# Kernel optimization log

Hardware: AMD Instinct MI355X
Metric: run time of the kernel (lower is better)

The kernel has to match this reference:

```python
import jax, jax.numpy as jnp
import numpy as np

NUM_ITER = 3
HEADS = 8
EPS = 1e-8

def _ln(x, g, b, eps=1e-5):
    mu = x.mean(-1, keepdims=True)
    var = ((x - mu) ** 2).mean(-1, keepdims=True)
    return (x - mu) * jax.lax.rsqrt(var + eps) * g + b

def setup_inputs() -> dict:
    key = jax.random.key(0)
    ks = jax.random.split(key, 10)
    B, Nkv, Din = 32, 4096, 256
    Nq, S, Hm = 16, 256, 512
    def xav(k, shape):
        lim = (6.0 / (shape[0] + shape[1])) ** 0.5
        return jax.random.uniform(k, shape, minval=-lim, maxval=lim, dtype=jnp.float32)
    return {
        "slots": jax.random.normal(ks[0], (Nq, S), dtype=jnp.float32),
        "inputs": jax.random.normal(ks[1], (B, Nkv, Din), dtype=jnp.float32),
        "norm_in_g": jnp.ones((Din,), jnp.float32), "norm_in_b": jnp.zeros((Din,), jnp.float32),
        "norm_slots_g": jnp.ones((S,), jnp.float32), "norm_slots_b": jnp.zeros((S,), jnp.float32),
        "norm_mlp_g": jnp.ones((S,), jnp.float32), "norm_mlp_b": jnp.zeros((S,), jnp.float32),
        "Wq": xav(ks[2], (S, S)), "Wk": xav(ks[3], (S, Din)), "Wv": xav(ks[4], (S, Din)),
        "gru_wih": xav(ks[5], (3 * S, S)),
        "gru_whh": jax.random.normal(ks[6], (3 * S, S), dtype=jnp.float32) * (1.0 / S ** 0.5),
        "gru_bih": jnp.zeros((3 * S,), jnp.float32), "gru_bhh": jnp.zeros((3 * S,), jnp.float32),
        "mlp_w1": xav(ks[7], (Hm, S)), "mlp_b1": jnp.zeros((Hm,), jnp.float32),
        "mlp_w2": xav(ks[8], (S, Hm)), "mlp_b2": jnp.zeros((S,), jnp.float32),
    }

def reference(slots, inputs, norm_in_g, norm_in_b, norm_slots_g, norm_slots_b,
              norm_mlp_g, norm_mlp_b, Wq, Wk, Wv, gru_wih, gru_whh, gru_bih, gru_bhh,
              mlp_w1, mlp_b1, mlp_w2, mlp_b2):
    B, Nkv, Din = inputs.shape
    Nq, S = slots.shape
    H = HEADS
    hd = S // H
    slots = jnp.broadcast_to(slots, (B, Nq, S))
    x = _ln(inputs, norm_in_g, norm_in_b)
    k = (x @ Wk.T).reshape(B, Nkv, H, hd).transpose(0, 2, 1, 3) * (hd ** -0.5)  # [B,H,Nkv,hd]
    v = (x @ Wv.T).reshape(B, Nkv, H, hd).transpose(0, 2, 1, 3)
    attn_vis = None
    for _ in range(NUM_ITER):
        slots_prev = slots
        s = _ln(slots, norm_slots_g, norm_slots_b)
        q = (s @ Wq.T).reshape(B, Nq, H, hd).transpose(0, 2, 1, 3)  # [B,H,Nq,hd]
        # logits [B,Nkv,H*Nq]; softmax jointly over heads and slots per key (slot-axis softmax)
        logits = jnp.einsum('bhkd,bhqd->bkhq', k, q).reshape(B, Nkv, H * Nq)
        attn = jax.nn.softmax(logits, axis=-1).reshape(B, Nkv, H, Nq).transpose(0, 2, 1, 3)  # [B,H,Nkv,Nq]
        attn_vis = attn.sum(1)  # [B,Nkv,Nq]
        attn_n = attn / (attn.sum(axis=2, keepdims=True) + EPS)  # normalize over keys
        updates = jnp.einsum('bhkq,bhkd->bqhd', attn_n, v).reshape(B, Nq, S)
        # GRUCell: gates order r,z,n
        xg = updates.reshape(-1, S)
        h = slots_prev.reshape(-1, S)
        gi = xg @ gru_wih.T + gru_bih
        gh = h @ gru_whh.T + gru_bhh
        ir, iz, inn = jnp.split(gi, 3, axis=-1)
        hr, hz, hn = jnp.split(gh, 3, axis=-1)
        r = jax.nn.sigmoid(ir + hr)
        z = jax.nn.sigmoid(iz + hz)
        n = jnp.tanh(inn + r * hn)
        slots = ((1.0 - z) * n + z * h).reshape(B, Nq, S)
        m = _ln(slots, norm_mlp_g, norm_mlp_b)
        slots = slots + (jax.nn.relu(m @ mlp_w1.T + mlp_b1) @ mlp_w2.T + mlp_b2)
    return (slots, attn_vis)
```

## Files before the change

### kernel.cpp

```cpp
#include <hip/hip_runtime.h>
#include <stdint.h>

typedef unsigned short u16;
typedef __attribute__((ext_vector_type(8))) _Float16 half8;
typedef __attribute__((ext_vector_type(4))) _Float16 half4;
typedef __attribute__((ext_vector_type(4))) float floatx4;

__device__ inline float bflo(unsigned u){ return __uint_as_float(u << 16); }
__device__ inline float bfhi(unsigned u){ return __uint_as_float(u & 0xffff0000u); }
__device__ inline float bf1(u16 v){ return __uint_as_float(((unsigned)v) << 16); }
__device__ inline u16 f2bf(float f){
  unsigned u = __float_as_uint(f);
  u += 0x7fffu + ((u >> 16) & 1u);
  return (u16)(u >> 16);
}
__device__ inline float dot8(uint4 w, float4 a, float4 b, float acc){
  acc = fmaf(bflo(w.x), a.x, acc); acc = fmaf(bfhi(w.x), a.y, acc);
  acc = fmaf(bflo(w.y), a.z, acc); acc = fmaf(bfhi(w.y), a.w, acc);
  acc = fmaf(bflo(w.z), b.x, acc); acc = fmaf(bfhi(w.z), b.y, acc);
  acc = fmaf(bflo(w.w), b.z, acc); acc = fmaf(bfhi(w.w), b.w, acc);
  return acc;
}

#define CW_SLOTS 0
#define CW_GIN   4096
#define CW_BIN   4352
#define CW_GS    4608
#define CW_BS    4864
#define CW_GM    5120
#define CW_BM    5376
#define CW_WQ    5632
#define CW_WK    71168
#define CW_WV    136704
#define CW_WIH   202240
#define CW_WHH   398848
#define CW_BIH   595456
#define CW_BHH   596224
#define CW_W1    596992
#define CW_B1    728064
#define CW_W2    728576
#define CW_B2    859648
#define CW_TOTAL 859904

__global__ void k_flag(const u16* __restrict__ probe, int* __restrict__ flag){
  int t = threadIdx.x;
  int bad = 0;
  #pragma unroll
  for (int i = 0; i < 4; i++){
    float x = bf1(probe[t + i * 256]);
    if (!(fabsf(x) < 1e6f)) bad = 1;
  }
  __shared__ int s;
  if (t == 0) s = 0;
  __syncthreads();
  if (bad) atomicOr(&s, 1);
  __syncthreads();
  if (t == 0) *flag = s;
}

struct CanonArgs { const void* p[18]; };

__global__ void k_canon(CanonArgs a, const int* __restrict__ flag, u16* __restrict__ cw){
  const int off[19] = {CW_SLOTS, CW_GIN, CW_BIN, CW_GS, CW_BS, CW_GM, CW_BM, CW_WQ,
                       CW_WK, CW_WV, CW_WIH, CW_WHH, CW_BIH, CW_BHH, CW_W1, CW_B1,
                       CW_W2, CW_B2, CW_TOTAL};
  int i = blockIdx.x * 256 + threadIdx.x;
  if (i >= CW_TOTAL) return;
  int f32m = *flag;
  int j = 0;
  while (i >= off[j + 1]) j++;
  int local = i - off[j];
  float v = f32m ? ((const float*)a.p[j])[local] : bf1(((const u16*)a.p[j])[local]);
  cw[i] = f2bf(v);
}

__global__ void k_init(const u16* __restrict__ cw, float* __restrict__ slots,
                       _Float16* __restrict__ wkvh)
{
  int idx = blockIdx.x * 256 + threadIdx.x;
  if (idx < 131072){
    float g = bf1(cw[CW_GIN + (idx & 255)]);
    wkvh[idx] = (_Float16)(bf1(cw[CW_WK + idx]) * g);
  } else {
    int i = idx - 131072;
    int d = i & 255;
    int q = (i >> 8) & 15;
    slots[i] = bf1(cw[CW_SLOTS + q * 256 + d]);
  }
}

__global__ void k_beta(const u16* __restrict__ cw, float* __restrict__ beta,
                       float* __restrict__ colsum){
  int c = blockIdx.x * 256 + threadIdx.x;
  if (c >= 512) return;
  float a = 0.f, s = 0.f;
  for (int d = 0; d < 256; d++){
    float w = bf1(cw[CW_WK + c * 256 + d]);
    a = fmaf(bf1(cw[CW_BIN + d]), w, a);
    s = fmaf(bf1(cw[CW_GIN + d]), w, s);
  }
  beta[c] = a;
  colsum[c] = s;
}

__global__ void k_zero(float* __restrict__ p, int n){
  int i = blockIdx.x * 256 + threadIdx.x;
  if (i < n) p[i] = 0.f;
}

__global__ __launch_bounds__(256) void k1_gemm(
    const void* __restrict__ inp, const int* __restrict__ flag,
    const float* __restrict__ beta, const float* __restrict__ colsum,
    const _Float16* __restrict__ wkvh, _Float16* __restrict__ kh, _Float16* __restrict__ vT)
{
  int f32m = *flag;
  int tid = threadIdx.x;
  int wv = tid >> 6, lane = tid & 63;
  int m16 = lane & 15, q4 = lane >> 4;
  int nb = blockIdx.y;
  long rowb0 = (long)blockIdx.x * 128;
  int colW = nb * 256 + wv * 64;

  __shared__ _Float16 vtile[256][72];

  half8 bfr[4][8];
  #pragma unroll
  for (int nt = 0; nt < 4; nt++)
    #pragma unroll
    for (int s = 0; s < 8; s++)
      bfr[nt][s] = *(const half8*)(wkvh + (colW + nt * 16 + m16) * 256 + s * 32 + q4 * 8);

  float bet[4], cs[4];
  #pragma unroll
  for (int nt = 0; nt < 4; nt++){
    bet[nt] = beta[colW + nt * 16 + m16];
    cs[nt]  = colsum[colW + nt * 16 + m16];
  }

  for (int rt = 0; rt < 8; rt++){
    long rowb = rowb0 + rt * 16;
    long myRow = rowb + m16;

    float sum = 0.f, sq = 0.f;
    half8 af[8];
    if (f32m){
      const float* rp = (const float*)inp + myRow * 256 + q4 * 8;
      #pragma unroll
      for (int s = 0; s < 8; s++){
        float4 x0 = *(const float4*)(rp + s * 32);
        float4 x1 = *(const float4*)(rp + s * 32 + 4);
        sum += x0.x + x0.y + x0.z + x0.w + x1.x + x1.y + x1.z + x1.w;
        sq = fmaf(x0.x, x0.x, sq); sq = fmaf(x0.y, x0.y, sq);
        sq = fmaf(x0.z, x0.z, sq); sq = fmaf(x0.w, x0.w, sq);
        sq = fmaf(x1.x, x1.x, sq); sq = fmaf(x1.y, x1.y, sq);
        sq = fmaf(x1.z, x1.z, sq); sq = fmaf(x1.w, x1.w, sq);
        af[s][0] = (_Float16)x0.x; af[s][1] = (_Float16)x0.y;
        af[s][2] = (_Float16)x0.z; af[s][3] = (_Float16)x0.w;
        af[s][4] = (_Float16)x1.x; af[s][5] = (_Float16)x1.y;
        af[s][6] = (_Float16)x1.z; af[s][7] = (_Float16)x1.w;
      }
    } else {
      const u16* rp = (const u16*)inp + myRow * 256 + q4 * 8;
      #pragma unroll
      for (int s = 0; s < 8; s++){
        uint4 xu = *(const uint4*)(rp + s * 32);
        unsigned xw[4] = {xu.x, xu.y, xu.z, xu.w};
        #pragma unroll
        for (int p = 0; p < 4; p++){
          float a = bflo(xw[p]), b = bfhi(xw[p]);
          sum += a + b; sq = fmaf(a, a, sq); sq = fmaf(b, b, sq);
          af[s][2*p]   = (_Float16)a;
          af[s][2*p+1] = (_Float16)b;
        }
      }
    }
    sum += __shfl_xor(sum, 16); sq += __shfl_xor(sq, 16);
    sum += __shfl_xor(sum, 32); sq += __shfl_xor(sq, 32);
    float mu = sum * (1.f/256.f);
    float rstd = rsqrtf(fmaf(-mu, mu, sq * (1.f/256.f)) + 1e-5f);

    floatx4 acc[4];
    #pragma unroll
    for (int nt = 0; nt < 4; nt++) acc[nt] = (floatx4)0.f;
    #pragma unroll
    for (int s = 0; s < 8; s++)
      #pragma unroll
      for (int nt = 0; nt < 4; nt++)
        acc[nt] = __builtin_amdgcn_mfma_f32_16x16x32_f16(af[s], bfr[nt][s], acc[nt], 0, 0, 0);

    float mur[4], rsr[4];
    #pragma unroll
    for (int r = 0; r < 4; r++){
      mur[r] = __shfl(mu,   q4 * 4 + r);
      rsr[r] = __shfl(rstd, q4 * 4 + r);
    }
    #pragma unroll
    for (int nt = 0; nt < 4; nt++)
      #pragma unroll
      for (int r = 0; r < 4; r++)
        acc[nt][r] = fmaf(rsr[r], fmaf(-mur[r], cs[nt], acc[nt][r]), bet[nt]);

    if (nb == 0){
      long crow = rowb + q4 * 4;
      #pragma unroll
      for (int nt = 0; nt < 4; nt++)
        #pragma unroll
        for (int r = 0; r < 4; r++)
          kh[(crow + r) * 256 + colW + nt * 16 + m16] = (_Float16)acc[nt][r];
    } else {
      int klocal = (rt & 3) * 16 + q4 * 4;
      #pragma unroll
      for (int nt = 0; nt < 4; nt++){
        int cv = (colW - 256) + nt * 16 + m16;
        half4 pk;
        pk[0] = (_Float16)acc[nt][0]; pk[1] = (_Float16)acc[nt][1];
        pk[2] = (_Float16)acc[nt][2]; pk[3] = (_Float16)acc[nt][3];
        *(half4*)&vtile[cv][klocal] = pk;
      }
      if ((rt & 3) == 3){
        __syncthreads();
        int b = (int)(rowb0 >> 12);
        int keyb = ((int)rowb0 & 4095) + (rt >> 2) * 64;
        int cvo = wv * 8 + (lane >> 3);
        int k8  = (lane & 7) * 8;
        #pragma unroll
        for (int pass = 0; pass < 8; pass++){
          int cv = pass * 32 + cvo;
          half8 vvv = *(const half8*)&vtile[cv][k8];
          *(half8*)(vT + ((long)b * 256 + cv) * 4096 + keyb + k8) = vvv;
        }
        __syncthreads();
      }
    }
  }
}

__global__ __launch_bounds__(256) void k2_q(
    const float* __restrict__ slots, const u16* __restrict__ cw, _Float16* __restrict__ qh)
{
  const u16* gq = cw + CW_GS;
  const u16* bq = cw + CW_BS;
  const u16* Wq = cw + CW_WQ;
  int row = blockIdx.x, tid = threadIdx.x;
  int wv = tid >> 6, lane = tid & 63;
  float x = slots[row * 256 + tid];
  float s = x, s2 = x * x;
  #pragma unroll
  for (int m = 1; m < 64; m <<= 1){ s += __shfl_xor(s, m); s2 += __shfl_xor(s2, m); }
  __shared__ float red[8];
  if (lane == 0){ red[wv] = s; red[4 + wv] = s2; }
  __syncthreads();
  float tot  = red[0] + red[1] + red[2] + red[3];
  float tot2 = red[4] + red[5] + red[6] + red[7];
  float mu = tot * (1.f/256.f);
  float rstd = rsqrtf(tot2 * (1.f/256.f) - mu * mu + 1e-5f);
  __shared__ float sln[256];
  sln[tid] = (x - mu) * rstd * bf1(gq[tid]) + bf1(bq[tid]);
  __syncthreads();
  const u16* wr = Wq + tid * 256;
  float a = 0.f;
  for (int k = 0; k < 256; k += 8){
    uint4 wu = *(const uint4*)(wr + k);
    float4 l0 = *(const float4*)(sln + k);
    float4 l1 = *(const float4*)(sln + k + 4);
    a = dot8(wu, l0, l1, a);
  }
  qh[row * 256 + tid] = (_Float16)(a * 0.17677669529663687f);
}

__global__ __launch_bounds__(256) void k3_attn(
    const _Float16* __restrict__ kh, const _Float16* __restrict__ vT,
    const _Float16* __restrict__ qh,
    float* __restrict__ denom, float* __restrict__ numer,
    void* __restrict__ out_base, const int* __restrict__ flag, int lastIter)
{
  int f32m = *flag;
  int tid = threadIdx.x;
  int wv = tid >> 6, lane = tid & 63;
  int m16 = lane & 15, q4 = lane >> 4;
  int b = blockIdx.y, chunk = blockIdx.x;
  __shared__ float lds_l[32 * 129];

  half8 qf[2];
  #pragma unroll
  for (int hh = 0; hh < 2; hh++){
    int h = wv * 2 + hh;
    qf[hh] = *(const half8*)(qh + (b * 16 + m16) * 256 + h * 32 + q4 * 8);
  }
  float pd[2] = {0.f, 0.f};
  floatx4 un[2][2];
  #pragma unroll
  for (int hh = 0; hh < 2; hh++)
    #pragma unroll
    for (int dt = 0; dt < 2; dt++) un[hh][dt] = (floatx4)0.f;

  floatx4 z4 = (floatx4)0.f;
  for (int g4 = 0; g4 < 8; g4++){
    int key0 = chunk * 256 + g4 * 32;
    #pragma unroll
    for (int sub = 0; sub < 2; sub++){
      long rowb = (long)b * 4096 + key0 + sub * 16;
      #pragma unroll
      for (int hh = 0; hh < 2; hh++){
        int h = wv * 2 + hh;
        half8 af = *(const half8*)(kh + (rowb + m16) * 256 + h * 32 + q4 * 8);
        floatx4 d = __builtin_amdgcn_mfma_f32_16x16x32_f16(af, qf[hh], z4, 0, 0, 0);
        #pragma unroll
        for (int r = 0; r < 4; r++)
          lds_l[(sub * 16 + q4 * 4 + r) * 129 + h * 16 + m16] = d[r];
      }
    }
    __syncthreads();
    {
      int qq = tid & 15;
      #pragma unroll
      for (int half_ = 0; half_ < 2; half_++){
        int kk = (tid >> 4) + half_ * 16;
        float l[8];
        #pragma unroll
        for (int h8 = 0; h8 < 8; h8++) l[h8] = lds_l[kk * 129 + h8 * 16 + qq];
        float M = l[0];
        #pragma unroll
        for (int h8 = 1; h8 < 8; h8++) M = fmaxf(M, l[h8]);
        #pragma unroll
        for (int msk = 1; msk < 16; msk <<= 1) M = fmaxf(M, __shfl_xor(M, msk));
        float p[8], sl = 0.f;
        #pragma unroll
        for (int h8 = 0; h8 < 8; h8++){ p[h8] = __expf(l[h8] - M); sl += p[h8]; }
        float St = sl;
        #pragma unroll
        for (int msk = 1; msk < 16; msk <<= 1) St += __shfl_xor(St, msk);
        float rS = 1.f / St;
        if (lastIter){
          float av = sl * rS;
          long idx = 131072 + ((long)b * 4096 + key0 + kk) * 16 + qq;
          if (f32m) ((float*)out_base)[idx] = av;
          else      ((u16*)out_base)[idx]   = f2bf(av);
        }
        #pragma unroll
        for (int h8 = 0; h8 < 8; h8++) lds_l[kk * 129 + h8 * 16 + qq] = p[h8] * rS;
      }
    }
    __syncthreads();
    #pragma unroll
    for (int hh = 0; hh < 2; hh++){
      int h = wv * 2 + hh;
      float pv[8];
      #pragma unroll
      for (int j = 0; j < 8; j++) pv[j] = lds_l[(q4 * 8 + j) * 129 + h * 16 + m16];
      float ps = 0.f;
      #pragma unroll
      for (int j = 0; j < 8; j++) ps += pv[j];
      pd[hh] += ps;
      half8 bfr;
      #pragma unroll
      for (int j = 0; j < 8; j++) bfr[j] = (_Float16)pv[j];
      #pragma unroll
      for (int dt = 0; dt < 2; dt++){
        half8 afr = *(const half8*)(vT + ((long)b * 256 + h * 32 + dt * 16 + m16) * 4096 + key0 + q4 * 8);
        un[hh][dt] = __builtin_amdgcn_mfma_f32_16x16x32_f16(afr, bfr, un[hh][dt], 0, 0, 0);
      }
    }
    __syncthreads();
  }
  #pragma unroll
  for (int hh = 0; hh < 2; hh++){
    int h = wv * 2 + hh;
    float t = pd[hh];
    t += __shfl_xor(t, 16); t += __shfl_xor(t, 32);
    if (q4 == 0) atomicAdd(&denom[(b * 8 + h) * 16 + m16], t);
    #pragma unroll
    for (int dt = 0; dt < 2; dt++)
      #pragma unroll
      for (int r = 0; r < 4; r++)
        atomicAdd(&numer[((b * 8 + h) * 16 + m16) * 32 + dt * 16 + q4 * 4 + r], un[hh][dt][r]);
  }
}

__global__ __launch_bounds__(256) void k4a_gru(
    const float* __restrict__ slots, const float* __restrict__ numer, const float* __restrict__ denom,
    const u16* __restrict__ cw, float* __restrict__ mid)
{
  const u16* wih = cw + CW_WIH;
  const u16* whh = cw + CW_WHH;
  const u16* bih = cw + CW_BIH;
  const u16* bhh = cw + CW_BHH;
  int jc = blockIdx.x, rg = blockIdx.y;
  int tid = threadIdx.x;
  __shared__ float u_s[8][256];
  __shared__ float h_s[8][256];
  {
    int hh = tid >> 5, dh = tid & 31;
    for (int i = 0; i < 8; i++){
      int row = rg * 8 + i;
      int b = row >> 4, slot = row & 15;
      float den = denom[(b * 8 + hh) * 16 + slot] + 1e-8f;
      u_s[i][tid] = numer[((b * 8 + hh) * 16 + slot) * 32 + dh] / den;
      h_s[i][tid] = slots[row * 256 + tid];
    }
  }
  __syncthreads();
  int rl = tid >> 5, jl = tid & 31;
  int j = jc * 32 + jl;
  int row = rg * 8 + rl;
  const u16* wir = wih + j * 256;
  const u16* wiz = wih + (256 + j) * 256;
  const u16* win = wih + (512 + j) * 256;
  const u16* whr = whh + j * 256;
  const u16* whz = whh + (256 + j) * 256;
  const u16* whn = whh + (512 + j) * 256;
  float air = 0, aiz = 0, ain = 0, ahr = 0, ahz = 0, ahn = 0;
  for (int k = 0; k < 256; k += 8){
    float4 u0 = *(const float4*)(&u_s[rl][k]);
    float4 u1 = *(const float4*)(&u_s[rl][k + 4]);
    float4 h0 = *(const float4*)(&h_s[rl][k]);
    float4 h1 = *(const float4*)(&h_s[rl][k + 4]);
    air = dot8(*(const uint4*)(wir + k), u0, u1, air);
    aiz = dot8(*(const uint4*)(wiz + k), u0, u1, aiz);
    ain = dot8(*(const uint4*)(win + k), u0, u1, ain);
    ahr = dot8(*(const uint4*)(whr + k), h0, h1, ahr);
    ahz = dot8(*(const uint4*)(whz + k), h0, h1, ahz);
    ahn = dot8(*(const uint4*)(whn + k), h0, h1, ahn);
  }
  float gr = air + bf1(bih[j])       + ahr + bf1(bhh[j]);
  float gz = aiz + bf1(bih[256 + j]) + ahz + bf1(bhh[256 + j]);
  float r = 1.f / (1.f + __expf(-gr));
  float z = 1.f / (1.f + __expf(-gz));
  float nn = tanhf(ain + bf1(bih[512 + j]) + r * (ahn + bf1(bhh[512 + j])));
  float h = h_s[rl][j];
  mid[row * 256 + j] = (1.f - z) * nn + z * h;
}

__global__ __launch_bounds__(256) void k4b_mlp(
    const float* __restrict__ mid, const u16* __restrict__ cw,
    float* __restrict__ slots, void* __restrict__ out_base,
    const int* __restrict__ flag, int lastIter)
{
  int f32m = *flag;
  const u16* gm = cw + CW_GM;
  const u16* bm = cw + CW_BM;
  const u16* w1 = cw + CW_W1;
  const u16* b1 = cw + CW_B1;
  const u16* w2 = cw + CW_W2;
  const u16* b2 = cw + CW_B2;
  int row = blockIdx.x, tid = threadIdx.x;
  int wv = tid >> 6, lane = tid & 63;
  float x = mid[row * 256 + tid];
  float s = x, s2 = x * x;
  #pragma unroll
  for (int m = 1; m < 64; m <<= 1){ s += __shfl_xor(s, m); s2 += __shfl_xor(s2, m); }
  __shared__ float red[8];
  if (lane == 0){ red[wv] = s; red[4 + wv] = s2; }
  __syncthreads();
  float tot  = red[0] + red[1] + red[2] + red[3];
  float tot2 = red[4] + red[5] + red[6] + red[7];
  float mu = tot * (1.f/256.f);
  float rstd = rsqrtf(tot2 * (1.f/256.f) - mu * mu + 1e-5f);
  __shared__ float ls[256];
  __shared__ float h1[512];
  ls[tid] = (x - mu) * rstd * bf1(gm[tid]) + bf1(bm[tid]);
  __syncthreads();
  const u16* w1a = w1 + tid * 256;
  const u16* w1b = w1 + (tid + 256) * 256;
  float a0 = 0.f, a1 = 0.f;
  for (int k = 0; k < 256; k += 8){
    float4 l0 = *(const float4*)(ls + k);
    float4 l1 = *(const float4*)(ls + k + 4);
    a0 = dot8(*(const uint4*)(w1a + k), l0, l1, a0);
    a1 = dot8(*(const uint4*)(w1b + k), l0, l1, a1);
  }
  h1[tid]       = fmaxf(a0 + bf1(b1[tid]), 0.f);
  h1[tid + 256] = fmaxf(a1 + bf1(b1[tid + 256]), 0.f);
  __syncthreads();
  const u16* w2r = w2 + tid * 512;
  float a = 0.f;
  for (int k = 0; k < 512; k += 8){
    float4 l0 = *(const float4*)(h1 + k);
    float4 l1 = *(const float4*)(h1 + k + 4);
    a = dot8(*(const uint4*)(w2r + k), l0, l1, a);
  }
  float res = x + a + bf1(b2[tid]);
  slots[row * 256 + tid] = res;
  if (lastIter){
    int idx = row * 256 + tid;
    if (f32m) ((float*)out_base)[idx] = res;
    else      ((u16*)out_base)[idx]   = f2bf(res);
  }
}

extern "C" void kernel_launch(void* const* d_in, const int* in_sizes, int n_in,
                              void* d_out, int out_size, void* d_ws, size_t ws_size,
                              hipStream_t stream)
{
  char* ws = (char*)d_ws;
  int*  flagp    = (int*)ws;
  u16*  cw       = (u16*)(ws + 256);
  _Float16* qh   = (_Float16*)(ws + 1720064);
  _Float16* wkvh = (_Float16*)(ws + 1982208);
  float* slots   = (float*)(ws + 2244352);
  float* mid     = (float*)(ws + 2768640);
  float* numer   = (float*)(ws + 3292928);
  float* denom   = (float*)(ws + 3817216);
  _Float16* kh   = (_Float16*)(ws + 3833600);
  _Float16* vT   = (_Float16*)(ws + 70942464);
  float*  beta   = (float*)(ws + 3817216);
  float*  colsum = beta + 512;

  CanonArgs ca;
  ca.p[0]  = d_in[0];   ca.p[1]  = d_in[2];   ca.p[2]  = d_in[3];
  ca.p[3]  = d_in[4];   ca.p[4]  = d_in[5];   ca.p[5]  = d_in[6];
  ca.p[6]  = d_in[7];   ca.p[7]  = d_in[8];   ca.p[8]  = d_in[9];
  ca.p[9]  = d_in[10];  ca.p[10] = d_in[11];  ca.p[11] = d_in[12];
  ca.p[12] = d_in[13];  ca.p[13] = d_in[14];  ca.p[14] = d_in[15];
  ca.p[15] = d_in[16];  ca.p[16] = d_in[17];  ca.p[17] = d_in[18];

  k_flag<<<1, 256, 0, stream>>>((const u16*)d_in[1], flagp);
  k_canon<<<(CW_TOTAL + 255) / 256, 256, 0, stream>>>(ca, flagp, cw);
  k_init<<<1024, 256, 0, stream>>>(cw, slots, wkvh);
  k_beta<<<2, 256, 0, stream>>>(cw, beta, colsum);
  k1_gemm<<<dim3(1024, 2), 256, 0, stream>>>(d_in[1], flagp, beta, colsum, wkvh, kh, vT);
  for (int it = 0; it < 3; it++){
    int last = (it == 2) ? 1 : 0;
    k2_q<<<512, 256, 0, stream>>>(slots, cw, qh);
    k_zero<<<528, 256, 0, stream>>>(numer, 135168);
    k3_attn<<<dim3(16, 32), 256, 0, stream>>>(kh, vT, qh, denom, numer, d_out, flagp, last);
    k4a_gru<<<dim3(8, 64), 256, 0, stream>>>(slots, numer, denom, cw, mid);
    k4b_mlp<<<512, 256, 0, stream>>>(mid, cw, slots, d_out, flagp, last);
  }
}
```

Before: 899.3 us.

## Restructure K/V projection GEMM with LDS weights, prefetch pipeline, blocked vT layout

The K/V projection kernel now stages the weight slice in shared memory, pre-swizzled into MFMA fragment order, instead of holding it in registers. Blocks grow to 512 threads over 512 rows, and each wave double-buffers its input row loads so the next tile's global loads overlap the current tile's MFMA work. The vT layout becomes key-blocked in groups of 64 keys, so V stores go straight to global memory without the LDS transpose and its barriers. The attention kernel's V read indexing is updated to match. The cost is 128KB of LDS per block, which limits occupancy, and more LDS traffic for the B fragments.

```diff
diff --git a/kernel.cpp b/kernel.cpp
--- a/kernel.cpp
+++ b/kernel.cpp
@@ -108,63 +108,57 @@
   if (i < n) p[i] = 0.f;
 }
 
-__global__ __launch_bounds__(256) void k1_gemm(
-    const void* __restrict__ inp, const int* __restrict__ flag,
-    const float* __restrict__ beta, const float* __restrict__ colsum,
-    const _Float16* __restrict__ wkvh, _Float16* __restrict__ kh, _Float16* __restrict__ vT)
-{
-  int f32m = *flag;
-  int tid = threadIdx.x;
-  int wv = tid >> 6, lane = tid & 63;
-  int m16 = lane & 15, q4 = lane >> 4;
-  int nb = blockIdx.y;
-  long rowb0 = (long)blockIdx.x * 128;
-  int colW = nb * 256 + wv * 64;
-
-  __shared__ _Float16 vtile[256][72];
-
-  half8 bfr[4][8];
-  #pragma unroll
-  for (int nt = 0; nt < 4; nt++)
-    #pragma unroll
-    for (int s = 0; s < 8; s++)
-      bfr[nt][s] = *(const half8*)(wkvh + (colW + nt * 16 + m16) * 256 + s * 32 + q4 * 8);
-
+template<int F32>
+__device__ __forceinline__ void k1_body(
+    const void* __restrict__ inp, const float* __restrict__ beta,
+    const float* __restrict__ colsum, const _Float16* __restrict__ Bl,
+    _Float16* __restrict__ kh, _Float16* __restrict__ vT,
+    int nb, long rowb0, int colW, int wc, int m16, int q4, int lane)
+{
+  constexpr int NR = F32 ? 16 : 8;
   float bet[4], cs[4];
   #pragma unroll
   for (int nt = 0; nt < 4; nt++){
     bet[nt] = beta[colW + nt * 16 + m16];
     cs[nt]  = colsum[colW + nt * 16 + m16];
   }
-
-  for (int rt = 0; rt < 8; rt++){
-    long rowb = rowb0 + rt * 16;
+  long vbase = ((long)(rowb0 >> 12)) * 64 * 256;
+
+  uint4 ra[NR], rb_[NR];
+
+  auto LOAD = [&](long rowb, uint4* r){
     long myRow = rowb + m16;
-
+    if (F32){
+      const uint4* rp = (const uint4*)((const float*)inp + myRow * 256 + q4 * 8);
+      #pragma unroll
+      for (int s = 0; s < 8; s++){ r[2*s] = rp[s*8]; r[2*s+1] = rp[s*8+1]; }
+    } else {
+      const uint4* rp = (const uint4*)((const u16*)inp + myRow * 256 + q4 * 8);
+      #pragma unroll
+      for (int s = 0; s < 8; s++) r[s] = rp[s*4];
+    }
+  };
+
+  auto PROCESS = [&](long rowb, uint4* r){
     float sum = 0.f, sq = 0.f;
     half8 af[8];
-    if (f32m){
-      const float* rp = (const float*)inp + myRow * 256 + q4 * 8;
+    if (F32){
       #pragma unroll
       for (int s = 0; s < 8; s++){
-        float4 x0 = *(const float4*)(rp + s * 32);
-        float4 x1 = *(const float4*)(rp + s * 32 + 4);
-        sum += x0.x + x0.y + x0.z + x0.w + x1.x + x1.y + x1.z + x1.w;
-        sq = fmaf(x0.x, x0.x, sq); sq = fmaf(x0.y, x0.y, sq);
-        sq = fmaf(x0.z, x0.z, sq); sq = fmaf(x0.w, x0.w, sq);
-        sq = fmaf(x1.x, x1.x, sq); sq = fmaf(x1.y, x1.y, sq);
-        sq = fmaf(x1.z, x1.z, sq); sq = fmaf(x1.w, x1.w, sq);
-        af[s][0] = (_Float16)x0.x; af[s][1] = (_Float16)x0.y;
-        af[s][2] = (_Float16)x0.z; af[s][3] = (_Float16)x0.w;
-        af[s][4] = (_Float16)x1.x; af[s][5] = (_Float16)x1.y;
-        af[s][6] = (_Float16)x1.z; af[s][7] = (_Float16)x1.w;
+        float x[8] = { __uint_as_float(r[2*s].x), __uint_as_float(r[2*s].y),
+                       __uint_as_float(r[2*s].z), __uint_as_float(r[2*s].w),
+                       __uint_as_float(r[2*s+1].x), __uint_as_float(r[2*s+1].y),
+                       __uint_as_float(r[2*s+1].z), __uint_as_float(r[2*s+1].w) };
+        #pragma unroll
+        for (int p = 0; p < 8; p++){
+          sum += x[p]; sq = fmaf(x[p], x[p], sq);
+          af[s][p] = (_Float16)x[p];
+        }
       }
     } else {
-      const u16* rp = (const u16*)inp + myRow * 256 + q4 * 8;
       #pragma unroll
       for (int s = 0; s < 8; s++){
-        uint4 xu = *(const uint4*)(rp + s * 32);
-        unsigned xw[4] = {xu.x, xu.y, xu.z, xu.w};
+        unsigned xw[4] = {r[s].x, r[s].y, r[s].z, r[s].w};
         #pragma unroll
         for (int p = 0; p < 4; p++){
           float a = bflo(xw[p]), b = bfhi(xw[p]);
@@ -185,54 +179,87 @@
     #pragma unroll
     for (int s = 0; s < 8; s++)
       #pragma unroll
-      for (int nt = 0; nt < 4; nt++)
-        acc[nt] = __builtin_amdgcn_mfma_f32_16x16x32_f16(af[s], bfr[nt][s], acc[nt], 0, 0, 0);
+      for (int nt = 0; nt < 4; nt++){
+        half8 bfr = *(const half8*)(Bl + (((wc * 4 + nt) * 8 + s) * 64 + lane) * 8);
+        acc[nt] = __builtin_amdgcn_mfma_f32_16x16x32_f16(af[s], bfr, acc[nt], 0, 0, 0);
+      }
 
     float mur[4], rsr[4];
     #pragma unroll
-    for (int r = 0; r < 4; r++){
-      mur[r] = __shfl(mu,   q4 * 4 + r);
-      rsr[r] = __shfl(rstd, q4 * 4 + r);
+    for (int r2 = 0; r2 < 4; r2++){
+      mur[r2] = __shfl(mu,   q4 * 4 + r2);
+      rsr[r2] = __shfl(rstd, q4 * 4 + r2);
     }
     #pragma unroll
     for (int nt = 0; nt < 4; nt++)
       #pragma unroll
-      for (int r = 0; r < 4; r++)
-        acc[nt][r] = fmaf(rsr[r], fmaf(-mur[r], cs[nt], acc[nt][r]), bet[nt]);
+      for (int r2 = 0; r2 < 4; r2++)
+        acc[nt][r2] = fmaf(rsr[r2], fmaf(-mur[r2], cs[nt], acc[nt][r2]), bet[nt]);
 
     if (nb == 0){
       long crow = rowb + q4 * 4;
       #pragma unroll
       for (int nt = 0; nt < 4; nt++)
         #pragma unroll
-        for (int r = 0; r < 4; r++)
-          kh[(crow + r) * 256 + colW + nt * 16 + m16] = (_Float16)acc[nt][r];
+        for (int r2 = 0; r2 < 4; r2++)
+          kh[(crow + r2) * 256 + colW + nt * 16 + m16] = (_Float16)acc[nt][r2];
     } else {
-      int klocal = (rt & 3) * 16 + q4 * 4;
+      int kloc = (int)rowb & 4095;
+      long kg = vbase + (long)(kloc >> 6) * 256;
+      int klo = (kloc & 63) + q4 * 4;
       #pragma unroll
       for (int nt = 0; nt < 4; nt++){
         int cv = (colW - 256) + nt * 16 + m16;
         half4 pk;
         pk[0] = (_Float16)acc[nt][0]; pk[1] = (_Float16)acc[nt][1];
         pk[2] = (_Float16)acc[nt][2]; pk[3] = (_Float16)acc[nt][3];
-        *(half4*)&vtile[cv][klocal] = pk;
-      }
-      if ((rt & 3) == 3){
-        __syncthreads();
-        int b = (int)(rowb0 >> 12);
-        int keyb = ((int)rowb0 & 4095) + (rt >> 2) * 64;
-        int cvo = wv * 8 + (lane >> 3);
-        int k8  = (lane & 7) * 8;
-        #pragma unroll
-        for (int pass = 0; pass < 8; pass++){
-          int cv = pass * 32 + cvo;
-          half8 vvv = *(const half8*)&vtile[cv][k8];
-          *(half8*)(vT + ((long)b * 256 + cv) * 4096 + keyb + k8) = vvv;
-        }
-        __syncthreads();
-      }
-    }
-  }
+        *(half4*)(vT + (kg + cv) * 64 + klo) = pk;
+      }
+    }
+  };
+
+  LOAD(rowb0, ra);
+  #pragma unroll 1
+  for (int rt = 0; rt < 16; rt += 2){
+    LOAD(rowb0 + (rt + 1) * 16, rb_);
+    PROCESS(rowb0 + rt * 16, ra);
+    if (rt + 2 < 16) LOAD(rowb0 + (rt + 2) * 16, ra);
+    PROCESS(rowb0 + (rt + 1) * 16, rb_);
+  }
+}
+
+__global__ __launch_bounds__(512, 2) void k1_gemm(
+    const void* __restrict__ inp, const int* __restrict__ flag,
+    const float* __restrict__ beta, const float* __restrict__ colsum,
+    const _Float16* __restrict__ wkvh, _Float16* __restrict__ kh, _Float16* __restrict__ vT)
+{
+  int tid = threadIdx.x;
+  int wv = tid >> 6, lane = tid & 63;
+  int m16 = lane & 15, q4 = lane >> 4;
+  int wc = wv & 3, wr = wv >> 2;
+  int nb = blockIdx.y;
+  long rowb0 = (long)blockIdx.x * 512 + wr * 256;
+  int colW = nb * 256 + wc * 64;
+
+  __shared__ _Float16 Bl[65536];
+
+  {
+    const _Float16* wb = wkvh + (long)nb * 65536;
+    #pragma unroll
+    for (int i = 0; i < 16; i++){
+      int f = i * 512 + tid;
+      int lf = f & 63;
+      int s  = (f >> 6) & 7;
+      int ntw = f >> 9;
+      int col = (ntw >> 2) * 64 + (ntw & 3) * 16 + (lf & 15);
+      int k8  = s * 32 + (lf >> 4) * 8;
+      *(half8*)(Bl + f * 8) = *(const half8*)(wb + col * 256 + k8);
+    }
+  }
+  __syncthreads();
+
+  if (*flag) k1_body<1>(inp, beta, colsum, Bl, kh, vT, nb, rowb0, colW, wc, m16, q4, lane);
+  else       k1_body<0>(inp, beta, colsum, Bl, kh, vT, nb, rowb0, colW, wc, m16, q4, lane);
 }
 
 __global__ __launch_bounds__(256) void k2_q(
@@ -342,6 +369,8 @@
       }
     }
     __syncthreads();
+    int kg0 = key0 >> 6;
+    int kr  = (key0 & 63) + q4 * 8;
     #pragma unroll
     for (int hh = 0; hh < 2; hh++){
       int h = wv * 2 + hh;
@@ -357,7 +386,7 @@
       for (int j = 0; j < 8; j++) bfr[j] = (_Float16)pv[j];
       #pragma unroll
       for (int dt = 0; dt < 2; dt++){
-        half8 afr = *(const half8*)(vT + ((long)b * 256 + h * 32 + dt * 16 + m16) * 4096 + key0 + q4 * 8);
+        half8 afr = *(const half8*)(vT + (((long)b * 64 + kg0) * 256 + h * 32 + dt * 16 + m16) * 64 + kr);
         un[hh][dt] = __builtin_amdgcn_mfma_f32_16x16x32_f16(afr, bfr, un[hh][dt], 0, 0, 0);
       }
     }
@@ -518,7 +547,7 @@
   k_canon<<<(CW_TOTAL + 255) / 256, 256, 0, stream>>>(ca, flagp, cw);
   k_init<<<1024, 256, 0, stream>>>(cw, slots, wkvh);
   k_beta<<<2, 256, 0, stream>>>(cw, beta, colsum);
-  k1_gemm<<<dim3(1024, 2), 256, 0, stream>>>(d_in[1], flagp, beta, colsum, wkvh, kh, vT);
+  k1_gemm<<<dim3(256, 2), 512, 0, stream>>>(d_in[1], flagp, beta, colsum, wkvh, kh, vT);
   for (int it = 0; it < 3; it++){
     int last = (it == 2) ? 1 : 0;
     k2_q<<<512, 256, 0, stream>>>(slots, cw, qh);
```

New measurement: 907.7 us. Within noise of the previous version (+0.9%).
